# Kernel optimization log

Measured on AMD Instinct MI355X. Metric: run time of the kernel, lower is better.

The kernel has to match this reference:

```python
import jax, jax.numpy as jnp
import numpy as np

B, S, D = 2, 2048, 2048
H, KV, DK = 16, 4, 128
G = H // KV  # GQA groups
EPS = 1e-6
BASE = 10000.0


def _rope_tables(seq_len, dim):
    inv_freq = 1.0 / (BASE ** (jnp.arange(0, dim, 2, dtype=jnp.float32) / dim))
    t = jnp.arange(seq_len, dtype=jnp.float32)
    freqs = t[:, None] * inv_freq[None, :]            # [S, dim/2]
    emb = jnp.concatenate([freqs, freqs], axis=-1)    # [S, dim]
    # broadcast over [b, s, h, d]
    return jnp.cos(emb)[None, :, None, :], jnp.sin(emb)[None, :, None, :]


def _rotate_half(x):
    x1, x2 = jnp.split(x, 2, axis=-1)
    return jnp.concatenate([-x2, x1], axis=-1)


def _rms_norm(x, w):
    return x * jax.lax.rsqrt(jnp.mean(x * x, axis=-1, keepdims=True) + EPS) * w


def setup_inputs() -> dict:
    key = jax.random.key(0)
    ks = jax.random.split(key, 5)
    std = 0.02
    return {
        "x": jax.random.normal(ks[0], (B, S, D), jnp.float32),
        "Wq": jax.random.normal(ks[1], (D, H * DK), jnp.float32) * std,
        "Wk": jax.random.normal(ks[2], (D, KV * DK), jnp.float32) * std,
        "Wv": jax.random.normal(ks[3], (D, KV * DK), jnp.float32) * std,
        "Wo": jax.random.normal(ks[4], (H * DK, D), jnp.float32) * std,
        "q_norm_w": jnp.ones((DK,), jnp.float32),
        "k_norm_w": jnp.ones((DK,), jnp.float32),
    }


def reference(x, Wq, Wk, Wv, Wo, q_norm_w, k_norm_w):
    b, s, d = x.shape
    q = (x @ Wq).reshape(b, s, H, DK)
    k = (x @ Wk).reshape(b, s, KV, DK)
    v = (x @ Wv).reshape(b, s, KV, DK)

    # per-head RMSNorm on q/k
    q = _rms_norm(q, q_norm_w)
    k = _rms_norm(k, k_norm_w)

    # RoPE (applied in [b, s, h, d] layout like the original)
    cos, sin = _rope_tables(s, DK)
    q = q * cos + _rotate_half(q) * sin
    k = k * cos + _rotate_half(k) * sin

    # GQA attention without materializing repeated K/V:
    # q: [b, kv, g, s, d];  k, v: [b, kv, s, d]
    q = q.transpose(0, 2, 1, 3).reshape(b, KV, G, s, DK)
    k = k.transpose(0, 2, 1, 3)
    v = v.transpose(0, 2, 1, 3)

    scale = 1.0 / np.sqrt(DK)
    scores = jnp.einsum('bkgqd,bkpd->bkgqp', q, k) * scale  # [b,kv,g,s,s]
    causal = jnp.tril(jnp.ones((s, s), dtype=bool))
    scores = jnp.where(causal, scores, jnp.finfo(scores.dtype).min)
    attn = jax.nn.softmax(scores, axis=-1)
    out = jnp.einsum('bkgqp,bkpd->bkgqd', attn, v)           # [b,kv,g,s,d]

    out = out.reshape(b, H, s, DK).transpose(0, 2, 1, 3).reshape(b, s, H * DK)
    return out @ Wo
```

## Files before the change

### kernel.cpp

```cpp
#include <hip/hip_runtime.h>

typedef __attribute__((ext_vector_type(4))) float f32x4;
typedef __attribute__((ext_vector_type(8))) short s16x8;

struct alignas(8) us4 { ushort x, y, z, w; };

__device__ __forceinline__ ushort f2bf(float f) {
  unsigned u = __builtin_bit_cast(unsigned, f);
  u += 0x7fffu + ((u >> 16) & 1u);
  return (ushort)(u >> 16);
}
__device__ __forceinline__ float bf2f(ushort h) {
  unsigned u = ((unsigned)h) << 16;
  return __builtin_bit_cast(float, u);
}

__device__ __forceinline__ void gload_lds16(const ushort* g, ushort* l) {
  __builtin_amdgcn_global_load_lds((const __attribute__((address_space(1))) unsigned int*)g,
                                   (__attribute__((address_space(3))) unsigned int*)l, 16, 0, 0);
}

__global__ __launch_bounds__(256) void preproc_kernel(
    const float* __restrict__ x, const float* __restrict__ Wq, const float* __restrict__ Wk,
    const float* __restrict__ Wv, const float* __restrict__ Wo,
    ushort* __restrict__ xb, ushort* __restrict__ WqkvT, ushort* __restrict__ WoT,
    float* __restrict__ rc, float* __restrict__ rs) {
  __shared__ float tile[32][33];
  int bid = blockIdx.x, tid = threadIdx.x;
  if (bid < 2048) {
    const int n4 = 4096 * 2048 / 4;
    for (int i = bid * 256 + tid; i < n4; i += 2048 * 256) {
      float4 v = reinterpret_cast<const float4*>(x)[i];
      us4 o;
      o.x = f2bf(v.x); o.y = f2bf(v.y); o.z = f2bf(v.z); o.w = f2bf(v.w);
      reinterpret_cast<us4*>(xb)[i] = o;
    }
  } else if (bid < 2560) {
    int t = (bid - 2048) * 4 + (tid >> 6), j = tid & 63;
    float inv = expf(-(float)j * (9.210340371976184f / 64.0f));
    float ang = (float)t * inv;
    float s, c;
    sincosf(ang, &s, &c);
    rc[t * 64 + j] = c;
    rs[t * 64 + j] = s;
  } else {
    int wid = bid - 2560;
    const float* src;
    ushort* dst;
    int C, bx, by;
    if (wid < 4096) { src = Wq; dst = WqkvT; C = 2048; bx = wid & 63; by = wid >> 6; }
    else if (wid < 5120) { int w2 = wid - 4096; src = Wk; dst = WqkvT + (size_t)2048 * 2048; C = 512; bx = w2 & 15; by = w2 >> 4; }
    else if (wid < 6144) { int w2 = wid - 5120; src = Wv; dst = WqkvT + (size_t)2560 * 2048; C = 512; bx = w2 & 15; by = w2 >> 4; }
    else { int w2 = wid - 6144; src = Wo; dst = WoT; C = 2048; bx = w2 & 63; by = w2 >> 6; }
    int c0 = bx * 32, r0 = by * 32;
    int tx = tid & 31, ty = tid >> 5;
#pragma unroll
    for (int i = 0; i < 4; ++i)
      tile[ty + i * 8][tx] = src[(size_t)(r0 + ty + i * 8) * C + c0 + tx];
    __syncthreads();
#pragma unroll
    for (int i = 0; i < 4; ++i)
      dst[(size_t)(c0 + ty + i * 8) * 2048 + r0 + tx] = f2bf(tile[tx][ty + i * 8]);
  }
}

__global__ __launch_bounds__(256) void postqkv_kernel(
    const ushort* __restrict__ qkv, const float* __restrict__ kw,
    ushort* __restrict__ Kb, ushort* __restrict__ vt,
    const float* __restrict__ rc, const float* __restrict__ rs) {
  __shared__ ushort tile[64][136];
  int bid = blockIdx.x, tid = threadIdx.x;
  if (bid < 4096) {
    int wv = tid >> 6, lane = tid & 63;
    int row = bid * 4 + wv;
    int token = row >> 2, head = row & 3;
    const ushort* p = qkv + (size_t)token * 3072 + 2048 + head * 128;
    float x1 = bf2f(p[lane]), x2 = bf2f(p[lane + 64]);
    float ss = x1 * x1 + x2 * x2;
#pragma unroll
    for (int m = 32; m > 0; m >>= 1) ss += __shfl_xor(ss, m);
    float r = rsqrtf(ss * (1.0f / 128.0f) + 1e-6f);
    float xn1 = x1 * r * kw[lane], xn2 = x2 * r * kw[lane + 64];
    int t = token & 2047;
    float c = rc[t * 64 + lane], s = rs[t * 64 + lane];
    ushort* o = Kb + (size_t)token * 512 + head * 128;
    o[lane] = f2bf(xn1 * c - xn2 * s);
    o[lane + 64] = f2bf(xn2 * c + xn1 * s);
  } else {
    int bx = bid - 4096;
    int st = bx & 31, kvh = (bx >> 5) & 3, b = bx >> 7;
    int s0 = st * 64;
#pragma unroll
    for (int p = 0; p < 4; ++p) {
      int idx = p * 2048 + tid * 8;
      int s = idx >> 7, d = idx & 127;
      *(s16x8*)&tile[s][d] =
          *(const s16x8*)&qkv[(size_t)(b * 2048 + s0 + s) * 3072 + 2560 + kvh * 128 + d];
    }
    __syncthreads();
#pragma unroll
    for (int p = 0; p < 4; ++p) {
      int idx = p * 2048 + tid * 8;
      int d = idx >> 6, s = idx & 63;
      s16x8 v;
#pragma unroll
      for (int u = 0; u < 8; ++u) v[u] = (short)tile[s + u][d];
      *(s16x8*)&vt[(size_t)((b * 4 + kvh) * 128 + d) * 2048 + s0 + s] = v;
    }
  }
}

template <bool OUTF32>
__global__ __launch_bounds__(512, 1) void gemm256sq_kernel(const ushort* __restrict__ A,
                                                           const ushort* __restrict__ Bt,
                                                           void* __restrict__ Cp,
                                                           int M, int N, int K) {
  __shared__ ushort As[2][256][64];
  __shared__ ushort Bs[2][256][64];
  int tid = threadIdx.x;
  int lane = tid & 63, wv = tid >> 6;
  int wm = wv >> 2, wn = wv & 3;
  int lr = lane & 15, lg = lane >> 4;
  int nwg = gridDim.x * gridDim.y;
  int flat = blockIdx.y * gridDim.x + blockIdx.x;
  int swz = (flat & 7) * (nwg >> 3) + (flat >> 3);
  int bx = swz % gridDim.x, by = swz / gridDim.x;
  int m0 = by * 256, n0 = bx * 256;
  int srow8 = lane >> 3;
  int gcol = ((lane & 7) * 8) ^ (srow8 << 3);
  int nt = K >> 6;

  const ushort* Abase = A + (size_t)m0 * K;
  const ushort* Bbase = Bt + (size_t)n0 * K;

  auto stage = [&](int slot, int t) {
#pragma unroll
    for (int p = 0; p < 4; ++p) {
      int r0 = wv * 32 + p * 8;
      gload_lds16(&Abase[(size_t)(r0 + srow8) * K + t * 64 + gcol], &As[slot][r0][0]);
    }
#pragma unroll
    for (int p = 0; p < 4; ++p) {
      int r0 = wv * 32 + p * 8;
      gload_lds16(&Bbase[(size_t)(r0 + srow8) * K + t * 64 + gcol], &Bs[slot][r0][0]);
    }
  };

  stage(0, 0);

  f32x4 acc[8][4] = {};
  int arow[8], aswz[8], brow[4], bswz[4];
#pragma unroll
  for (int i = 0; i < 8; ++i) {
    arow[i] = wm * 128 + i * 16 + lr;
    aswz[i] = (arow[i] & 7) << 3;
  }
#pragma unroll
  for (int j = 0; j < 4; ++j) {
    brow[j] = wn * 64 + j * 16 + lr;
    bswz[j] = (brow[j] & 7) << 3;
  }

  for (int t = 0; t < nt; ++t) {
    int c = t & 1;
    if (t + 1 < nt) {
      stage(c ^ 1, t + 1);
      asm volatile("s_waitcnt vmcnt(8)" ::: "memory");
    } else {
      asm volatile("s_waitcnt vmcnt(0)" ::: "memory");
    }
    __builtin_amdgcn_s_barrier();
#pragma unroll
    for (int ks = 0; ks < 2; ++ks) {
      s16x8 a[8], b[4];
#pragma unroll
      for (int i = 0; i < 8; ++i)
        a[i] = *(const s16x8*)&As[c][arow[i]][(ks * 32 + lg * 8) ^ aswz[i]];
#pragma unroll
      for (int j = 0; j < 4; ++j)
        b[j] = *(const s16x8*)&Bs[c][brow[j]][(ks * 32 + lg * 8) ^ bswz[j]];
      __builtin_amdgcn_s_setprio(1);
#pragma unroll
      for (int i = 0; i < 8; ++i)
#pragma unroll
        for (int j = 0; j < 4; ++j)
          acc[i][j] = __builtin_amdgcn_mfma_f32_16x16x32_bf16(a[i], b[j], acc[i][j], 0, 0, 0);
      __builtin_amdgcn_s_setprio(0);
    }
    __builtin_amdgcn_s_barrier();
  }
#pragma unroll
  for (int i = 0; i < 8; ++i)
#pragma unroll
    for (int j = 0; j < 4; ++j) {
      int row = m0 + wm * 128 + i * 16 + lg * 4;
      int col = n0 + wn * 64 + j * 16 + lr;
#pragma unroll
      for (int r = 0; r < 4; ++r) {
        float v = acc[i][j][r];
        if (OUTF32)
          reinterpret_cast<float*>(Cp)[(size_t)(row + r) * N + col] = v;
        else
          reinterpret_cast<ushort*>(Cp)[(size_t)(row + r) * N + col] = f2bf(v);
      }
    }
}

template <bool OUTF32>
__global__ __launch_bounds__(512, 2) void gemm256_kernel(const ushort* __restrict__ A,
                                                         const ushort* __restrict__ Bt,
                                                         void* __restrict__ Cp,
                                                         int M, int N, int K) {
  __shared__ ushort As[3][256][64];
  __shared__ ushort Bs[3][128][64];
  int tid = threadIdx.x;
  int lane = tid & 63, wv = tid >> 6;
  int wm = wv >> 1, wn = wv & 1;
  int lr = lane & 15, lg = lane >> 4;
  int nwg = gridDim.x * gridDim.y;
  int flat = blockIdx.y * gridDim.x + blockIdx.x;
  int swz = (flat & 7) * (nwg >> 3) + (flat >> 3);
  int bx = swz % gridDim.x, by = swz / gridDim.x;
  int m0 = by * 256, n0 = bx * 128;
  int srow8 = lane >> 3;
  int gcol = ((lane & 7) * 8) ^ (srow8 << 3);
  int nt = K >> 6;

  const ushort* Abase = A + (size_t)m0 * K;
  const ushort* Bbase = Bt + (size_t)n0 * K;

  auto stageA = [&](int slot, int t, int p) {
    int r0 = (wv * 4 + p) * 8;
    gload_lds16(&Abase[(size_t)(r0 + srow8) * K + t * 64 + gcol], &As[slot][r0][0]);
  };
  auto stageB = [&](int slot, int t, int p) {
    int r0 = (wv * 2 + p) * 8;
    gload_lds16(&Bbase[(size_t)(r0 + srow8) * K + t * 64 + gcol], &Bs[slot][r0][0]);
  };

  stageA(0, 0, 0); stageA(0, 0, 1); stageB(0, 0, 0);
  stageA(0, 0, 2); stageA(0, 0, 3); stageB(0, 0, 1);
  stageA(1, 1, 0); stageA(1, 1, 1); stageB(1, 1, 0);
  stageA(1, 1, 2); stageA(1, 1, 3); stageB(1, 1, 1);

  f32x4 acc[4][4] = {};
  int arow[4], brow[4], aswz[4], bswz[4];
#pragma unroll
  for (int i = 0; i < 4; ++i) {
    arow[i] = wm * 64 + i * 16 + lr;
    aswz[i] = (arow[i] & 7) << 3;
    brow[i] = wn * 64 + i * 16 + lr;
    bswz[i] = (brow[i] & 7) << 3;
  }

  for (int t = 0; t < nt; ++t) {
    int cur = t % 3, pf = (t + 2) % 3;
    if (t + 1 < nt) {
      asm volatile("s_waitcnt vmcnt(6)" ::: "memory");
    } else {
      asm volatile("s_waitcnt vmcnt(0)" ::: "memory");
    }
    __builtin_amdgcn_s_barrier();
    bool do_pf = (t + 2) < nt;
    {
      s16x8 a[4], b[4];
#pragma unroll
      for (int i = 0; i < 4; ++i) a[i] = *(const s16x8*)&As[cur][arow[i]][(lg * 8) ^ aswz[i]];
#pragma unroll
      for (int j = 0; j < 4; ++j) b[j] = *(const s16x8*)&Bs[cur][brow[j]][(lg * 8) ^ bswz[j]];
      if (do_pf) { stageA(pf, t + 2, 0); stageA(pf, t + 2, 1); stageB(pf, t + 2, 0); }
      __builtin_amdgcn_s_setprio(1);
#pragma unroll
      for (int i = 0; i < 4; ++i)
#pragma unroll
        for (int j = 0; j < 4; ++j)
          acc[i][j] = __builtin_amdgcn_mfma_f32_16x16x32_bf16(a[i], b[j], acc[i][j], 0, 0, 0);
      __builtin_amdgcn_s_setprio(0);
    }
    {
      s16x8 a[4], b[4];
#pragma unroll
      for (int i = 0; i < 4; ++i) a[i] = *(const s16x8*)&As[cur][arow[i]][(32 + lg * 8) ^ aswz[i]];
#pragma unroll
      for (int j = 0; j < 4; ++j) b[j] = *(const s16x8*)&Bs[cur][brow[j]][(32 + lg * 8) ^ bswz[j]];
      if (do_pf) { stageA(pf, t + 2, 2); stageA(pf, t + 2, 3); stageB(pf, t + 2, 1); }
      __builtin_amdgcn_s_setprio(1);
#pragma unroll
      for (int i = 0; i < 4; ++i)
#pragma unroll
        for (int j = 0; j < 4; ++j)
          acc[i][j] = __builtin_amdgcn_mfma_f32_16x16x32_bf16(a[i], b[j], acc[i][j], 0, 0, 0);
      __builtin_amdgcn_s_setprio(0);
    }
  }
#pragma unroll
  for (int i = 0; i < 4; ++i)
#pragma unroll
    for (int j = 0; j < 4; ++j) {
      int row = m0 + wm * 64 + i * 16 + lg * 4;
      int col = n0 + wn * 64 + j * 16 + lr;
#pragma unroll
      for (int r = 0; r < 4; ++r) {
        float v = acc[i][j][r];
        if (OUTF32)
          reinterpret_cast<float*>(Cp)[(size_t)(row + r) * N + col] = v;
        else
          reinterpret_cast<ushort*>(Cp)[(size_t)(row + r) * N + col] = f2bf(v);
      }
    }
}

__global__ __launch_bounds__(256, 2) void attn_kernel(const ushort* __restrict__ QKV,
                                                      const ushort* __restrict__ Kn,
                                                      const ushort* __restrict__ Vt,
                                                      ushort* __restrict__ AO,
                                                      const float* __restrict__ rc,
                                                      const float* __restrict__ rs,
                                                      const float* __restrict__ qw) {
  __shared__ ushort Ks[2][64][128];
  __shared__ ushort Vs[2][128][64];
  __shared__ ushort Ps[4][32][64];
  int bxi = blockIdx.x;
  int g = bxi >> 5, bh = bxi & 31;
  int qt = (g < 8) ? (15 - g) : (g - 8);
  int b = bh >> 4, h = bh & 15, kvh = h >> 2;
  int q0 = qt * 128;
  int nt = 2 * qt + 2;
  int tid = threadIdx.x, lane = tid & 63, w = tid >> 6;
  int lr = lane & 15, lg = lane >> 4;

  int ksrow = lane >> 4, kscol = (lane & 15) * 8;
  int vsrow = lane >> 3, vscol = (lane & 7) * 8;

  auto stage = [&](int c, int t) {
    int p0 = t * 64;
#pragma unroll
    for (int p = 0; p < 4; ++p) {
      int r0 = w * 16 + p * 4;
      int row = r0 + ksrow;
      int gc = kscol ^ ((row & 7) << 3);
      gload_lds16(&Kn[(size_t)(b * 2048 + p0 + row) * 512 + kvh * 128 + gc], &Ks[c][r0][0]);
    }
#pragma unroll
    for (int p = 0; p < 4; ++p) {
      int r0 = w * 32 + p * 8;
      int row = r0 + vsrow;
      int gc = vscol ^ ((row & 7) << 3);
      gload_lds16(&Vt[(size_t)((b * 4 + kvh) * 128 + row) * 2048 + p0 + gc], &Vs[c][r0][0]);
    }
  };

  stage(0, 0);

  const float QSCALE = 0.12751744f;
  s16x8 qf[2][4];
#pragma unroll
  for (int qa = 0; qa < 2; ++qa) {
    int t_tok = q0 + w * 32 + qa * 16 + lr;
    const ushort* qp = QKV + (size_t)(b * 2048 + t_tok) * 3072 + h * 128;
    float xv[4][8];
    float ss = 0.f;
#pragma unroll
    for (int ks = 0; ks < 4; ++ks) {
      s16x8 raw = *(const s16x8*)&qp[ks * 32 + lg * 8];
#pragma unroll
      for (int j = 0; j < 8; ++j) {
        float x = bf2f((ushort)raw[j]);
        xv[ks][j] = x;
        ss += x * x;
      }
    }
    ss += __shfl_xor(ss, 16);
    ss += __shfl_xor(ss, 32);
    float rms = rsqrtf(ss * (1.0f / 128.0f) + 1e-6f);
#pragma unroll
    for (int ks = 0; ks < 2; ++ks) {
      int dbase = ks * 32 + lg * 8;
      float cc[8], sn[8], w1[8], w2[8];
      *(float4*)&cc[0] = *(const float4*)&rc[(size_t)t_tok * 64 + dbase];
      *(float4*)&cc[4] = *(const float4*)&rc[(size_t)t_tok * 64 + dbase + 4];
      *(float4*)&sn[0] = *(const float4*)&rs[(size_t)t_tok * 64 + dbase];
      *(float4*)&sn[4] = *(const float4*)&rs[(size_t)t_tok * 64 + dbase + 4];
      *(float4*)&w1[0] = *(const float4*)&qw[dbase];
      *(float4*)&w1[4] = *(const float4*)&qw[dbase + 4];
      *(float4*)&w2[0] = *(const float4*)&qw[dbase + 64];
      *(float4*)&w2[4] = *(const float4*)&qw[dbase + 68];
      s16x8 o1, o2;
#pragma unroll
      for (int j = 0; j < 8; ++j) {
        float x1 = xv[ks][j] * rms * w1[j];
        float x2 = xv[ks + 2][j] * rms * w2[j];
        o1[j] = (short)f2bf((x1 * cc[j] - x2 * sn[j]) * QSCALE);
        o2[j] = (short)f2bf((x2 * cc[j] + x1 * sn[j]) * QSCALE);
      }
      qf[qa][ks] = o1;
      qf[qa][ks + 2] = o2;
    }
  }

  f32x4 O[2][8] = {};
  float mrow[2] = {-1e30f, -1e30f};
  float lrow[2] = {0.f, 0.f};

  for (int t = 0; t < nt; ++t) {
    int c = t & 1;
    if (t + 1 < nt) {
      stage(c ^ 1, t + 1);
      asm volatile("s_waitcnt vmcnt(8)" ::: "memory");
    } else {
      asm volatile("s_waitcnt vmcnt(0)" ::: "memory");
    }
    __builtin_amdgcn_s_barrier();

    bool skip = (t == 2 * qt + 1) && (w < 2);
    if (!skip) {
      f32x4 sacc[2][4] = {};
      __builtin_amdgcn_s_setprio(1);
#pragma unroll
      for (int ks = 0; ks < 4; ++ks) {
        s16x8 bk[4];
#pragma unroll
        for (int fp = 0; fp < 4; ++fp) {
          int kr = fp * 16 + lr;
          bk[fp] = *(const s16x8*)&Ks[c][kr][(ks * 32 + lg * 8) ^ ((kr & 7) << 3)];
        }
#pragma unroll
        for (int qa = 0; qa < 2; ++qa)
#pragma unroll
          for (int fp = 0; fp < 4; ++fp)
            sacc[qa][fp] = __builtin_amdgcn_mfma_f32_16x16x32_bf16(bk[fp], qf[qa][ks], sacc[qa][fp], 0, 0, 0);
      }
      __builtin_amdgcn_s_setprio(0);

      if (t >= 2 * qt) {
        int p0 = t * 64;
#pragma unroll
        for (int qa = 0; qa < 2; ++qa)
#pragma unroll
          for (int fp = 0; fp < 4; ++fp)
#pragma unroll
            for (int r = 0; r < 4; ++r) {
              int qg = q0 + w * 32 + qa * 16 + lr;
              int pg = p0 + fp * 16 + lg * 4 + r;
              if (pg > qg) sacc[qa][fp][r] = -1e30f;
            }
      }

      float pml[2];
#pragma unroll
      for (int qa = 0; qa < 2; ++qa) {
        float m0 = fmaxf(fmaxf(sacc[qa][0][0], sacc[qa][0][1]), fmaxf(sacc[qa][0][2], sacc[qa][0][3]));
        float m1 = fmaxf(fmaxf(sacc[qa][1][0], sacc[qa][1][1]), fmaxf(sacc[qa][1][2], sacc[qa][1][3]));
        float m2 = fmaxf(fmaxf(sacc[qa][2][0], sacc[qa][2][1]), fmaxf(sacc[qa][2][2], sacc[qa][2][3]));
        float m3 = fmaxf(fmaxf(sacc[qa][3][0], sacc[qa][3][1]), fmaxf(sacc[qa][3][2], sacc[qa][3][3]));
        pml[qa] = fmaxf(fmaxf(m0, m1), fmaxf(m2, m3));
      }
      bool need = (pml[0] > mrow[0] + 8.0f) | (pml[1] > mrow[1] + 8.0f);
      if (__any((int)need)) {
        float fsc[2];
#pragma unroll
        for (int qa = 0; qa < 2; ++qa) {
          float pm = fmaxf(pml[qa], __shfl_xor(pml[qa], 16));
          pm = fmaxf(pm, __shfl_xor(pm, 32));
          float mn = fmaxf(mrow[qa], pm);
          fsc[qa] = __builtin_amdgcn_exp2f(mrow[qa] - mn);
          mrow[qa] = mn;
          lrow[qa] *= fsc[qa];
        }
#pragma unroll
        for (int qa = 0; qa < 2; ++qa) {
          float fo[4];
#pragma unroll
          for (int r = 0; r < 4; ++r) fo[r] = __shfl(fsc[qa], lg * 4 + r);
#pragma unroll
          for (int fn = 0; fn < 8; ++fn)
#pragma unroll
            for (int r = 0; r < 4; ++r) O[qa][fn][r] *= fo[r];
        }
      }
#pragma unroll
      for (int qa = 0; qa < 2; ++qa) {
        float ls = 0.f;
        int prow = qa * 16 + lr;
        int swz = (lr & 7) << 3;
#pragma unroll
        for (int fp = 0; fp < 4; ++fp) {
          float e0 = __builtin_amdgcn_exp2f(sacc[qa][fp][0] - mrow[qa]);
          float e1 = __builtin_amdgcn_exp2f(sacc[qa][fp][1] - mrow[qa]);
          float e2 = __builtin_amdgcn_exp2f(sacc[qa][fp][2] - mrow[qa]);
          float e3 = __builtin_amdgcn_exp2f(sacc[qa][fp][3] - mrow[qa]);
          ls += (e0 + e1) + (e2 + e3);
          unsigned lo = (unsigned)f2bf(e0) | ((unsigned)f2bf(e1) << 16);
          unsigned hi = (unsigned)f2bf(e2) | ((unsigned)f2bf(e3) << 16);
          uint2 pk; pk.x = lo; pk.y = hi;
          *reinterpret_cast<uint2*>(&Ps[w][prow][(fp * 16 + lg * 4) ^ swz]) = pk;
        }
        lrow[qa] += ls;
      }
      __builtin_amdgcn_s_setprio(1);
#pragma unroll
      for (int ks2 = 0; ks2 < 2; ++ks2) {
        s16x8 ap[2];
#pragma unroll
        for (int qa = 0; qa < 2; ++qa) {
          int prow = qa * 16 + lr;
          ap[qa] = *(const s16x8*)&Ps[w][prow][(ks2 * 32 + lg * 8) ^ ((lr & 7) << 3)];
        }
#pragma unroll
        for (int fn = 0; fn < 8; ++fn) {
          int vrow = fn * 16 + lr;
          s16x8 bv = *(const s16x8*)&Vs[c][vrow][(ks2 * 32 + lg * 8) ^ ((vrow & 7) << 3)];
#pragma unroll
          for (int qa = 0; qa < 2; ++qa)
            O[qa][fn] = __builtin_amdgcn_mfma_f32_16x16x32_bf16(ap[qa], bv, O[qa][fn], 0, 0, 0);
        }
      }
      __builtin_amdgcn_s_setprio(0);
    }
    __builtin_amdgcn_s_barrier();
  }

#pragma unroll
  for (int qa = 0; qa < 2; ++qa) {
    lrow[qa] += __shfl_xor(lrow[qa], 16);
    lrow[qa] += __shfl_xor(lrow[qa], 32);
  }
#pragma unroll
  for (int qa = 0; qa < 2; ++qa) {
    float inv = 1.0f / lrow[qa];
    float invq[4];
#pragma unroll
    for (int r = 0; r < 4; ++r) invq[r] = __shfl(inv, lg * 4 + r);
#pragma unroll
    for (int fn = 0; fn < 8; ++fn)
#pragma unroll
      for (int r = 0; r < 4; ++r) {
        size_t idx = (size_t)(b * 2048 + q0 + w * 32 + qa * 16 + lg * 4 + r) * 2048 +
                     h * 128 + fn * 16 + lr;
        AO[idx] = f2bf(O[qa][fn][r] * invq[r]);
      }
  }
}

extern "C" void kernel_launch(void* const* d_in, const int* in_sizes, int n_in,
                              void* d_out, int out_size, void* d_ws, size_t ws_size,
                              hipStream_t stream) {
  (void)in_sizes; (void)n_in; (void)out_size; (void)ws_size;
  const float* x = (const float*)d_in[0];
  const float* Wq = (const float*)d_in[1];
  const float* Wk = (const float*)d_in[2];
  const float* Wv = (const float*)d_in[3];
  const float* Wo = (const float*)d_in[4];
  const float* qw = (const float*)d_in[5];
  const float* kw = (const float*)d_in[6];
  float* out = (float*)d_out;

  char* ws = (char*)d_ws;
  size_t off = 0;
  auto alloc = [&](size_t bytes) {
    void* p = ws + off;
    off += (bytes + 255) & ~(size_t)255;
    return p;
  };
  ushort* xb = (ushort*)alloc((size_t)4096 * 2048 * 2);
  ushort* WqkvT = (ushort*)alloc((size_t)3072 * 2048 * 2);
  ushort* WoT = (ushort*)alloc((size_t)2048 * 2048 * 2);
  ushort* QKVraw = (ushort*)alloc((size_t)4096 * 3072 * 2);
  ushort* Kb = (ushort*)alloc((size_t)4096 * 512 * 2);
  ushort* Vt = (ushort*)alloc((size_t)4096 * 512 * 2);
  ushort* AO = (ushort*)alloc((size_t)4096 * 2048 * 2);
  float* rc = (float*)alloc((size_t)2048 * 64 * 4);
  float* rs = (float*)alloc((size_t)2048 * 64 * 4);

  preproc_kernel<<<12800, 256, 0, stream>>>(x, Wq, Wk, Wv, Wo, xb, WqkvT, WoT, rc, rs);
  gemm256sq_kernel<false><<<dim3(12, 16), 512, 0, stream>>>(xb, WqkvT, QKVraw, 4096, 3072, 2048);
  postqkv_kernel<<<4352, 256, 0, stream>>>(QKVraw, kw, Kb, Vt, rc, rs);
  attn_kernel<<<512, 256, 0, stream>>>(QKVraw, Kb, Vt, AO, rc, rs, qw);
  gemm256_kernel<true><<<dim3(16, 16), 512, 0, stream>>>(AO, WoT, out, 4096, 2048, 2048);
}
```

Measured before the change: 198.9 us.

## Load K/V fragments directly from global memory instead of LDS double-buffering

The attention kernel no longer stages K and V tiles into shared memory with async global-to-LDS loads and barriers. Each wave now reads its MFMA operand fragments straight from global memory (relying on L1/L2 caching), and the launch bound is raised to 4 blocks per CU to exploit the reduced LDS footprint. This removes the block-wide barriers and LDS traffic but makes the four waves each fetch the same K/V data redundantly, with no prefetch overlap, exposing global-load latency inside the MFMA loops.

```diff
diff --git a/kernel.cpp b/kernel.cpp
--- a/kernel.cpp
+++ b/kernel.cpp
@@ -310,15 +310,13 @@
     }
 }
 
-__global__ __launch_bounds__(256, 2) void attn_kernel(const ushort* __restrict__ QKV,
+__global__ __launch_bounds__(256, 4) void attn_kernel(const ushort* __restrict__ QKV,
                                                       const ushort* __restrict__ Kn,
                                                       const ushort* __restrict__ Vt,
                                                       ushort* __restrict__ AO,
                                                       const float* __restrict__ rc,
                                                       const float* __restrict__ rs,
                                                       const float* __restrict__ qw) {
-  __shared__ ushort Ks[2][64][128];
-  __shared__ ushort Vs[2][128][64];
   __shared__ ushort Ps[4][32][64];
   int bxi = blockIdx.x;
   int g = bxi >> 5, bh = bxi & 31;
@@ -328,29 +326,6 @@
   int nt = 2 * qt + 2;
   int tid = threadIdx.x, lane = tid & 63, w = tid >> 6;
   int lr = lane & 15, lg = lane >> 4;
-
-  int ksrow = lane >> 4, kscol = (lane & 15) * 8;
-  int vsrow = lane >> 3, vscol = (lane & 7) * 8;
-
-  auto stage = [&](int c, int t) {
-    int p0 = t * 64;
-#pragma unroll
-    for (int p = 0; p < 4; ++p) {
-      int r0 = w * 16 + p * 4;
-      int row = r0 + ksrow;
-      int gc = kscol ^ ((row & 7) << 3);
-      gload_lds16(&Kn[(size_t)(b * 2048 + p0 + row) * 512 + kvh * 128 + gc], &Ks[c][r0][0]);
-    }
-#pragma unroll
-    for (int p = 0; p < 4; ++p) {
-      int r0 = w * 32 + p * 8;
-      int row = r0 + vsrow;
-      int gc = vscol ^ ((row & 7) << 3);
-      gload_lds16(&Vt[(size_t)((b * 4 + kvh) * 128 + row) * 2048 + p0 + gc], &Vs[c][r0][0]);
-    }
-  };
-
-  stage(0, 0);
 
   const float QSCALE = 0.12751744f;
   s16x8 qf[2][4];
@@ -398,126 +373,116 @@
     }
   }
 
+  const ushort* Kbase = Kn + (size_t)(b * 2048 + lr) * 512 + kvh * 128 + lg * 8;
+  const ushort* Vbase = Vt + (size_t)((b * 4 + kvh) * 128 + lr) * 2048 + lg * 8;
+
   f32x4 O[2][8] = {};
   float mrow[2] = {-1e30f, -1e30f};
   float lrow[2] = {0.f, 0.f};
 
   for (int t = 0; t < nt; ++t) {
-    int c = t & 1;
-    if (t + 1 < nt) {
-      stage(c ^ 1, t + 1);
-      asm volatile("s_waitcnt vmcnt(8)" ::: "memory");
-    } else {
-      asm volatile("s_waitcnt vmcnt(0)" ::: "memory");
-    }
-    __builtin_amdgcn_s_barrier();
-
+    int p0 = t * 64;
     bool skip = (t == 2 * qt + 1) && (w < 2);
-    if (!skip) {
-      f32x4 sacc[2][4] = {};
-      __builtin_amdgcn_s_setprio(1);
-#pragma unroll
-      for (int ks = 0; ks < 4; ++ks) {
-        s16x8 bk[4];
-#pragma unroll
-        for (int fp = 0; fp < 4; ++fp) {
-          int kr = fp * 16 + lr;
-          bk[fp] = *(const s16x8*)&Ks[c][kr][(ks * 32 + lg * 8) ^ ((kr & 7) << 3)];
-        }
+    if (skip) continue;
+
+    f32x4 sacc[2][4] = {};
+    __builtin_amdgcn_s_setprio(1);
+#pragma unroll
+    for (int ks = 0; ks < 4; ++ks) {
+      s16x8 bk[4];
+#pragma unroll
+      for (int fp = 0; fp < 4; ++fp)
+        bk[fp] = *(const s16x8*)&Kbase[(size_t)(p0 + fp * 16) * 512 + ks * 32];
+#pragma unroll
+      for (int qa = 0; qa < 2; ++qa)
+#pragma unroll
+        for (int fp = 0; fp < 4; ++fp)
+          sacc[qa][fp] = __builtin_amdgcn_mfma_f32_16x16x32_bf16(bk[fp], qf[qa][ks], sacc[qa][fp], 0, 0, 0);
+    }
+    __builtin_amdgcn_s_setprio(0);
+
+    if (t >= 2 * qt) {
+#pragma unroll
+      for (int qa = 0; qa < 2; ++qa)
+#pragma unroll
+        for (int fp = 0; fp < 4; ++fp)
+#pragma unroll
+          for (int r = 0; r < 4; ++r) {
+            int qg = q0 + w * 32 + qa * 16 + lr;
+            int pg = p0 + fp * 16 + lg * 4 + r;
+            if (pg > qg) sacc[qa][fp][r] = -1e30f;
+          }
+    }
+
+    float pml[2];
+#pragma unroll
+    for (int qa = 0; qa < 2; ++qa) {
+      float m0 = fmaxf(fmaxf(sacc[qa][0][0], sacc[qa][0][1]), fmaxf(sacc[qa][0][2], sacc[qa][0][3]));
+      float m1 = fmaxf(fmaxf(sacc[qa][1][0], sacc[qa][1][1]), fmaxf(sacc[qa][1][2], sacc[qa][1][3]));
+      float m2 = fmaxf(fmaxf(sacc[qa][2][0], sacc[qa][2][1]), fmaxf(sacc[qa][2][2], sacc[qa][2][3]));
+      float m3 = fmaxf(fmaxf(sacc[qa][3][0], sacc[qa][3][1]), fmaxf(sacc[qa][3][2], sacc[qa][3][3]));
+      pml[qa] = fmaxf(fmaxf(m0, m1), fmaxf(m2, m3));
+    }
+    bool need = (pml[0] > mrow[0] + 8.0f) | (pml[1] > mrow[1] + 8.0f);
+    if (__any((int)need)) {
+      float fsc[2];
+#pragma unroll
+      for (int qa = 0; qa < 2; ++qa) {
+        float pm = fmaxf(pml[qa], __shfl_xor(pml[qa], 16));
+        pm = fmaxf(pm, __shfl_xor(pm, 32));
+        float mn = fmaxf(mrow[qa], pm);
+        fsc[qa] = __builtin_amdgcn_exp2f(mrow[qa] - mn);
+        mrow[qa] = mn;
+        lrow[qa] *= fsc[qa];
+      }
+#pragma unroll
+      for (int qa = 0; qa < 2; ++qa) {
+        float fo[4];
+#pragma unroll
+        for (int r = 0; r < 4; ++r) fo[r] = __shfl(fsc[qa], lg * 4 + r);
+#pragma unroll
+        for (int fn = 0; fn < 8; ++fn)
+#pragma unroll
+          for (int r = 0; r < 4; ++r) O[qa][fn][r] *= fo[r];
+      }
+    }
+#pragma unroll
+    for (int qa = 0; qa < 2; ++qa) {
+      float ls = 0.f;
+      int prow = qa * 16 + lr;
+      int swz = (lr & 7) << 3;
+#pragma unroll
+      for (int fp = 0; fp < 4; ++fp) {
+        float e0 = __builtin_amdgcn_exp2f(sacc[qa][fp][0] - mrow[qa]);
+        float e1 = __builtin_amdgcn_exp2f(sacc[qa][fp][1] - mrow[qa]);
+        float e2 = __builtin_amdgcn_exp2f(sacc[qa][fp][2] - mrow[qa]);
+        float e3 = __builtin_amdgcn_exp2f(sacc[qa][fp][3] - mrow[qa]);
+        ls += (e0 + e1) + (e2 + e3);
+        unsigned lo = (unsigned)f2bf(e0) | ((unsigned)f2bf(e1) << 16);
+        unsigned hi = (unsigned)f2bf(e2) | ((unsigned)f2bf(e3) << 16);
+        uint2 pk; pk.x = lo; pk.y = hi;
+        *reinterpret_cast<uint2*>(&Ps[w][prow][(fp * 16 + lg * 4) ^ swz]) = pk;
+      }
+      lrow[qa] += ls;
+    }
+    __builtin_amdgcn_s_setprio(1);
+#pragma unroll
+    for (int ks2 = 0; ks2 < 2; ++ks2) {
+      s16x8 ap[2];
+#pragma unroll
+      for (int qa = 0; qa < 2; ++qa) {
+        int prow = qa * 16 + lr;
+        ap[qa] = *(const s16x8*)&Ps[w][prow][(ks2 * 32 + lg * 8) ^ ((lr & 7) << 3)];
+      }
+#pragma unroll
+      for (int fn = 0; fn < 8; ++fn) {
+        s16x8 bv = *(const s16x8*)&Vbase[(size_t)(fn * 16) * 2048 + p0 + ks2 * 32];
 #pragma unroll
         for (int qa = 0; qa < 2; ++qa)
-#pragma unroll
-          for (int fp = 0; fp < 4; ++fp)
-            sacc[qa][fp] = __builtin_amdgcn_mfma_f32_16x16x32_bf16(bk[fp], qf[qa][ks], sacc[qa][fp], 0, 0, 0);
-      }
-      __builtin_amdgcn_s_setprio(0);
-
-      if (t >= 2 * qt) {
-        int p0 = t * 64;
-#pragma unroll
-        for (int qa = 0; qa < 2; ++qa)
-#pragma unroll
-          for (int fp = 0; fp < 4; ++fp)
-#pragma unroll
-            for (int r = 0; r < 4; ++r) {
-              int qg = q0 + w * 32 + qa * 16 + lr;
-              int pg = p0 + fp * 16 + lg * 4 + r;
-              if (pg > qg) sacc[qa][fp][r] = -1e30f;
-            }
-      }
-
-      float pml[2];
-#pragma unroll
-      for (int qa = 0; qa < 2; ++qa) {
-        float m0 = fmaxf(fmaxf(sacc[qa][0][0], sacc[qa][0][1]), fmaxf(sacc[qa][0][2], sacc[qa][0][3]));
-        float m1 = fmaxf(fmaxf(sacc[qa][1][0], sacc[qa][1][1]), fmaxf(sacc[qa][1][2], sacc[qa][1][3]));
-        float m2 = fmaxf(fmaxf(sacc[qa][2][0], sacc[qa][2][1]), fmaxf(sacc[qa][2][2], sacc[qa][2][3]));
-        float m3 = fmaxf(fmaxf(sacc[qa][3][0], sacc[qa][3][1]), fmaxf(sacc[qa][3][2], sacc[qa][3][3]));
-        pml[qa] = fmaxf(fmaxf(m0, m1), fmaxf(m2, m3));
-      }
-      bool need = (pml[0] > mrow[0] + 8.0f) | (pml[1] > mrow[1] + 8.0f);
-      if (__any((int)need)) {
-        float fsc[2];
-#pragma unroll
-        for (int qa = 0; qa < 2; ++qa) {
-          float pm = fmaxf(pml[qa], __shfl_xor(pml[qa], 16));
-          pm = fmaxf(pm, __shfl_xor(pm, 32));
-          float mn = fmaxf(mrow[qa], pm);
-          fsc[qa] = __builtin_amdgcn_exp2f(mrow[qa] - mn);
-          mrow[qa] = mn;
-          lrow[qa] *= fsc[qa];
-        }
-#pragma unroll
-        for (int qa = 0; qa < 2; ++qa) {
-          float fo[4];
-#pragma unroll
-          for (int r = 0; r < 4; ++r) fo[r] = __shfl(fsc[qa], lg * 4 + r);
-#pragma unroll
-          for (int fn = 0; fn < 8; ++fn)
-#pragma unroll
-            for (int r = 0; r < 4; ++r) O[qa][fn][r] *= fo[r];
-        }
-      }
-#pragma unroll
-      for (int qa = 0; qa < 2; ++qa) {
-        float ls = 0.f;
-        int prow = qa * 16 + lr;
-        int swz = (lr & 7) << 3;
-#pragma unroll
-        for (int fp = 0; fp < 4; ++fp) {
-          float e0 = __builtin_amdgcn_exp2f(sacc[qa][fp][0] - mrow[qa]);
-          float e1 = __builtin_amdgcn_exp2f(sacc[qa][fp][1] - mrow[qa]);
-          float e2 = __builtin_amdgcn_exp2f(sacc[qa][fp][2] - mrow[qa]);
-          float e3 = __builtin_amdgcn_exp2f(sacc[qa][fp][3] - mrow[qa]);
-          ls += (e0 + e1) + (e2 + e3);
-          unsigned lo = (unsigned)f2bf(e0) | ((unsigned)f2bf(e1) << 16);
-          unsigned hi = (unsigned)f2bf(e2) | ((unsigned)f2bf(e3) << 16);
-          uint2 pk; pk.x = lo; pk.y = hi;
-          *reinterpret_cast<uint2*>(&Ps[w][prow][(fp * 16 + lg * 4) ^ swz]) = pk;
-        }
-        lrow[qa] += ls;
-      }
-      __builtin_amdgcn_s_setprio(1);
-#pragma unroll
-      for (int ks2 = 0; ks2 < 2; ++ks2) {
-        s16x8 ap[2];
-#pragma unroll
-        for (int qa = 0; qa < 2; ++qa) {
-          int prow = qa * 16 + lr;
-          ap[qa] = *(const s16x8*)&Ps[w][prow][(ks2 * 32 + lg * 8) ^ ((lr & 7) << 3)];
-        }
-#pragma unroll
-        for (int fn = 0; fn < 8; ++fn) {
-          int vrow = fn * 16 + lr;
-          s16x8 bv = *(const s16x8*)&Vs[c][vrow][(ks2 * 32 + lg * 8) ^ ((vrow & 7) << 3)];
-#pragma unroll
-          for (int qa = 0; qa < 2; ++qa)
-            O[qa][fn] = __builtin_amdgcn_mfma_f32_16x16x32_bf16(ap[qa], bv, O[qa][fn], 0, 0, 0);
-        }
-      }
-      __builtin_amdgcn_s_setprio(0);
-    }
-    __builtin_amdgcn_s_barrier();
+          O[qa][fn] = __builtin_amdgcn_mfma_f32_16x16x32_bf16(ap[qa], bv, O[qa][fn], 0, 0, 0);
+      }
+    }
+    __builtin_amdgcn_s_setprio(0);
   }
 
 #pragma unroll
```

After: 395.9 us. 99.0% more time.
